# Kernel tuning notes

Hardware: AMD Instinct MI355X
Metric: run time of the kernel (lower is better)

The kernel has to match this reference:

```python
import jax, jax.numpy as jnp
import numpy as np

T, B = 8192, 4096
NEG_SLOPE = 0.01


def setup_inputs() -> dict:
    key = jax.random.key(0)
    k1, k2 = jax.random.split(key)
    input_seq = jax.random.randint(k1, (T, B), 0, 2, dtype=jnp.int32)
    delta = jax.random.normal(k2, (2,), dtype=jnp.float32)
    return {"input_seq": input_seq, "delta": delta}


def reference(input_seq, delta):
    # Per-step: counter += delta[inp]; output = leaky_relu(counter).
    # counter itself is never clamped, so this is exactly
    # leaky_relu(cumsum(delta[input_seq], axis=time)).
    steps = delta[input_seq]                 # [T, B] gather from 2-entry table
    counter = jnp.cumsum(steps, axis=0)      # [T, B] prefix sum over time
    return jnp.where(counter >= 0, counter, NEG_SLOPE * counter)
```

## Files before the change

### kernel.cpp

```cpp
#include <hip/hip_runtime.h>
#include <stdint.h>

#define T_DIM 8192
#define B_DIM 4096
#define WORDS (T_DIM / 32)
#define NSEG 16
#define CTILE 256
#define NEG_SLOPE 0.01f

__global__ __launch_bounds__(1024) void ka_pack(const int* __restrict__ in,
                                                uint32_t* __restrict__ bits,
                                                int* __restrict__ segTotal) {
    const int c4  = threadIdx.x & 63;
    const int rc  = threadIdx.x >> 6;
    const int col0 = blockIdx.x * CTILE + c4 * 4;
    const int wordrow = blockIdx.y * 16 + rc;
    const int row0 = wordrow * 32;

    const int4* __restrict__ inv = (const int4*)in;
    uint32_t b0 = 0, b1 = 0, b2 = 0, b3 = 0;
#pragma unroll
    for (int r = 0; r < 32; ++r) {
        int4 v = inv[((size_t)(row0 + r) * B_DIM + col0) >> 2];
        b0 |= ((uint32_t)v.x & 1u) << r;
        b1 |= ((uint32_t)v.y & 1u) << r;
        b2 |= ((uint32_t)v.z & 1u) << r;
        b3 |= ((uint32_t)v.w & 1u) << r;
    }

    ((uint4*)bits)[((size_t)wordrow * B_DIM + col0) >> 2] = make_uint4(b0, b1, b2, b3);

    __shared__ int4 lds[16 * 64];
    lds[rc * 64 + c4] = make_int4(__popc(b0), __popc(b1), __popc(b2), __popc(b3));
    __syncthreads();

    if (rc == 0) {
        int4 s = make_int4(0, 0, 0, 0);
#pragma unroll
        for (int i = 0; i < 16; ++i) {
            int4 v = lds[i * 64 + c4];
            s.x += v.x; s.y += v.y; s.z += v.z; s.w += v.w;
        }
        ((int4*)segTotal)[((size_t)blockIdx.y * B_DIM + col0) >> 2] = s;
    }
}

__global__ __launch_bounds__(1024) void kb_emit(const uint32_t* __restrict__ bits,
                                                const int* __restrict__ segTotal,
                                                const float* __restrict__ delta,
                                                float* __restrict__ out) {
    const int c4  = threadIdx.x & 63;
    const int rc  = threadIdx.x >> 6;
    const int col0 = blockIdx.x * CTILE + c4 * 4;
    const int seg = blockIdx.y;
    const int wordrow = seg * 16 + rc;
    const int row0 = wordrow * 32;

    uint4 w = ((const uint4*)bits)[((size_t)wordrow * B_DIM + col0) >> 2];

    __shared__ int4 lds[16 * 64];
    lds[rc * 64 + c4] = make_int4(__popc(w.x), __popc(w.y), __popc(w.z), __popc(w.w));

    int c0 = 0, c1 = 0, c2 = 0, c3 = 0;
    for (int s = 0; s < seg; ++s) {
        int4 v = ((const int4*)segTotal)[((size_t)s * B_DIM + col0) >> 2];
        c0 += v.x; c1 += v.y; c2 += v.z; c3 += v.w;
    }
    __syncthreads();

    for (int i = 0; i < rc; ++i) {
        int4 v = lds[i * 64 + c4];
        c0 += v.x; c1 += v.y; c2 += v.z; c3 += v.w;
    }

    const float d0 = delta[0];
    const float dd = delta[1] - d0;

    float4* __restrict__ outv = (float4*)out;
#pragma unroll
    for (int r = 0; r < 32; ++r) {
        const int t = row0 + r;
        const float tp = (float)(t + 1) * d0;
        c0 += (int)((w.x >> r) & 1u);
        c1 += (int)((w.y >> r) & 1u);
        c2 += (int)((w.z >> r) & 1u);
        c3 += (int)((w.w >> r) & 1u);
        float4 o;
        o.x = fmaf((float)c0, dd, tp);
        o.y = fmaf((float)c1, dd, tp);
        o.z = fmaf((float)c2, dd, tp);
        o.w = fmaf((float)c3, dd, tp);
        o.x = (o.x >= 0.0f) ? o.x : NEG_SLOPE * o.x;
        o.y = (o.y >= 0.0f) ? o.y : NEG_SLOPE * o.y;
        o.z = (o.z >= 0.0f) ? o.z : NEG_SLOPE * o.z;
        o.w = (o.w >= 0.0f) ? o.w : NEG_SLOPE * o.w;
        outv[((size_t)t * B_DIM + col0) >> 2] = o;
    }
}

extern "C" void kernel_launch(void* const* d_in, const int* in_sizes, int n_in,
                              void* d_out, int out_size, void* d_ws, size_t ws_size,
                              hipStream_t stream) {
    const int*   in    = (const int*)d_in[0];
    const float* delta = (const float*)d_in[1];
    float*       out   = (float*)d_out;

    uint32_t* bits     = (uint32_t*)d_ws;
    int*      segTotal = (int*)((char*)d_ws + (size_t)WORDS * B_DIM * 4);

    dim3 grid(B_DIM / CTILE, NSEG);
    dim3 block(1024);

    hipLaunchKernelGGL(ka_pack, grid, block, 0, stream, in, bits, segTotal);
    hipLaunchKernelGGL(kb_emit, grid, block, 0, stream, bits, segTotal, delta, out);
}
```

Measured before the change: 242.0 us.

## Fuse pack and emit kernels into one cooperative kernel with grid sync

```diff
diff --git a/kernel.cpp b/kernel.cpp
--- a/kernel.cpp
+++ b/kernel.cpp
@@ -1,20 +1,25 @@
 #include <hip/hip_runtime.h>
+#include <hip/hip_cooperative_groups.h>
 #include <stdint.h>
+
+namespace cg = cooperative_groups;
 
 #define T_DIM 8192
 #define B_DIM 4096
-#define WORDS (T_DIM / 32)
 #define NSEG 16
 #define CTILE 256
 #define NEG_SLOPE 0.01f
 
-__global__ __launch_bounds__(1024) void ka_pack(const int* __restrict__ in,
-                                                uint32_t* __restrict__ bits,
-                                                int* __restrict__ segTotal) {
+__global__ __launch_bounds__(1024, 1) void fused_counter(
+        const int* __restrict__ in,
+        const float* __restrict__ delta,
+        float* __restrict__ out,
+        int* __restrict__ segTotal) {
     const int c4  = threadIdx.x & 63;
     const int rc  = threadIdx.x >> 6;
     const int col0 = blockIdx.x * CTILE + c4 * 4;
-    const int wordrow = blockIdx.y * 16 + rc;
+    const int seg = blockIdx.y;
+    const int wordrow = seg * 16 + rc;
     const int row0 = wordrow * 32;
 
     const int4* __restrict__ inv = (const int4*)in;
@@ -28,8 +33,6 @@
         b3 |= ((uint32_t)v.w & 1u) << r;
     }
 
-    ((uint4*)bits)[((size_t)wordrow * B_DIM + col0) >> 2] = make_uint4(b0, b1, b2, b3);
-
     __shared__ int4 lds[16 * 64];
     lds[rc * 64 + c4] = make_int4(__popc(b0), __popc(b1), __popc(b2), __popc(b3));
     __syncthreads();
@@ -41,33 +44,16 @@
             int4 v = lds[i * 64 + c4];
             s.x += v.x; s.y += v.y; s.z += v.z; s.w += v.w;
         }
-        ((int4*)segTotal)[((size_t)blockIdx.y * B_DIM + col0) >> 2] = s;
+        ((int4*)segTotal)[((size_t)seg * B_DIM + col0) >> 2] = s;
     }
-}
 
-__global__ __launch_bounds__(1024) void kb_emit(const uint32_t* __restrict__ bits,
-                                                const int* __restrict__ segTotal,
-                                                const float* __restrict__ delta,
-                                                float* __restrict__ out) {
-    const int c4  = threadIdx.x & 63;
-    const int rc  = threadIdx.x >> 6;
-    const int col0 = blockIdx.x * CTILE + c4 * 4;
-    const int seg = blockIdx.y;
-    const int wordrow = seg * 16 + rc;
-    const int row0 = wordrow * 32;
-
-    uint4 w = ((const uint4*)bits)[((size_t)wordrow * B_DIM + col0) >> 2];
-
-    __shared__ int4 lds[16 * 64];
-    lds[rc * 64 + c4] = make_int4(__popc(w.x), __popc(w.y), __popc(w.z), __popc(w.w));
+    cg::this_grid().sync();
 
     int c0 = 0, c1 = 0, c2 = 0, c3 = 0;
     for (int s = 0; s < seg; ++s) {
         int4 v = ((const int4*)segTotal)[((size_t)s * B_DIM + col0) >> 2];
         c0 += v.x; c1 += v.y; c2 += v.z; c3 += v.w;
     }
-    __syncthreads();
-
     for (int i = 0; i < rc; ++i) {
         int4 v = lds[i * 64 + c4];
         c0 += v.x; c1 += v.y; c2 += v.z; c3 += v.w;
@@ -81,10 +67,10 @@
     for (int r = 0; r < 32; ++r) {
         const int t = row0 + r;
         const float tp = (float)(t + 1) * d0;
-        c0 += (int)((w.x >> r) & 1u);
-        c1 += (int)((w.y >> r) & 1u);
-        c2 += (int)((w.z >> r) & 1u);
-        c3 += (int)((w.w >> r) & 1u);
+        c0 += (int)((b0 >> r) & 1u);
+        c1 += (int)((b1 >> r) & 1u);
+        c2 += (int)((b2 >> r) & 1u);
+        c3 += (int)((b3 >> r) & 1u);
         float4 o;
         o.x = fmaf((float)c0, dd, tp);
         o.y = fmaf((float)c1, dd, tp);
@@ -104,13 +90,11 @@
     const int*   in    = (const int*)d_in[0];
     const float* delta = (const float*)d_in[1];
     float*       out   = (float*)d_out;
-
-    uint32_t* bits     = (uint32_t*)d_ws;
-    int*      segTotal = (int*)((char*)d_ws + (size_t)WORDS * B_DIM * 4);
+    int*         segTotal = (int*)d_ws;
 
     dim3 grid(B_DIM / CTILE, NSEG);
     dim3 block(1024);
 
-    hipLaunchKernelGGL(ka_pack, grid, block, 0, stream, in, bits, segTotal);
-    hipLaunchKernelGGL(kb_emit, grid, block, 0, stream, bits, segTotal, delta, out);
+    void* args[] = { (void*)&in, (void*)&delta, (void*)&out, (void*)&segTotal };
+    hipLaunchCooperativeKernel((void*)fused_counter, grid, block, args, 0, stream);
 }
```

Measured after the change: 363.7 us. +50.3%, slower.

## Split each bit-word across two threads, double segments, use nontemporal loads/stores

Applied to the files above, without the earlier changes.

```diff
diff --git a/kernel.cpp b/kernel.cpp
--- a/kernel.cpp
+++ b/kernel.cpp
@@ -3,63 +3,80 @@
 
 #define T_DIM 8192
 #define B_DIM 4096
-#define WORDS (T_DIM / 32)
-#define NSEG 16
+#define NSEG 32
 #define CTILE 256
 #define NEG_SLOPE 0.01f
 
-__global__ __launch_bounds__(1024) void ka_pack(const int* __restrict__ in,
-                                                uint32_t* __restrict__ bits,
-                                                int* __restrict__ segTotal) {
-    const int c4  = threadIdx.x & 63;
-    const int rc  = threadIdx.x >> 6;
+typedef int   ivec4 __attribute__((ext_vector_type(4)));
+typedef float fvec4 __attribute__((ext_vector_type(4)));
+
+
+__global__ __launch_bounds__(1024, 8) void ka_pack(const int* __restrict__ in,
+                                                   uint32_t* __restrict__ bits,
+                                                   int* __restrict__ segTotal) {
+    const int c4   = threadIdx.x & 63;
+    const int rr   = threadIdx.x >> 6;
+    const int wl   = rr >> 1;
+    const int half = rr & 1;
     const int col0 = blockIdx.x * CTILE + c4 * 4;
-    const int wordrow = blockIdx.y * 16 + rc;
-    const int row0 = wordrow * 32;
+    const int wordrow = blockIdx.y * 8 + wl;
+    const int row0 = wordrow * 32 + half * 16;
 
-    const int4* __restrict__ inv = (const int4*)in;
+    const ivec4* __restrict__ inv = (const ivec4*)in;
     uint32_t b0 = 0, b1 = 0, b2 = 0, b3 = 0;
 #pragma unroll
-    for (int r = 0; r < 32; ++r) {
-        int4 v = inv[((size_t)(row0 + r) * B_DIM + col0) >> 2];
+    for (int r = 0; r < 16; ++r) {
+        ivec4 v = __builtin_nontemporal_load(&inv[((size_t)(row0 + r) * B_DIM + col0) >> 2]);
         b0 |= ((uint32_t)v.x & 1u) << r;
         b1 |= ((uint32_t)v.y & 1u) << r;
         b2 |= ((uint32_t)v.z & 1u) << r;
         b3 |= ((uint32_t)v.w & 1u) << r;
     }
 
-    ((uint4*)bits)[((size_t)wordrow * B_DIM + col0) >> 2] = make_uint4(b0, b1, b2, b3);
-
-    __shared__ int4 lds[16 * 64];
-    lds[rc * 64 + c4] = make_int4(__popc(b0), __popc(b1), __popc(b2), __popc(b3));
+    __shared__ uint4 halves[16][64];
+    __shared__ int4  cnts[8][64];
+    halves[rr][c4] = make_uint4(b0, b1, b2, b3);
     __syncthreads();
 
-    if (rc == 0) {
+    if (half == 0) {
+        uint4 lo = halves[rr][c4];
+        uint4 hi = halves[rr + 1][c4];
+        uint4 w = make_uint4(lo.x | (hi.x << 16), lo.y | (hi.y << 16),
+                             lo.z | (hi.z << 16), lo.w | (hi.w << 16));
+        ((uint4*)bits)[((size_t)wordrow * B_DIM + col0) >> 2] = w;
+        cnts[wl][c4] = make_int4(__popc(w.x), __popc(w.y), __popc(w.z), __popc(w.w));
+    }
+    __syncthreads();
+
+    if (rr == 0) {
         int4 s = make_int4(0, 0, 0, 0);
 #pragma unroll
-        for (int i = 0; i < 16; ++i) {
-            int4 v = lds[i * 64 + c4];
+        for (int i = 0; i < 8; ++i) {
+            int4 v = cnts[i][c4];
             s.x += v.x; s.y += v.y; s.z += v.z; s.w += v.w;
         }
         ((int4*)segTotal)[((size_t)blockIdx.y * B_DIM + col0) >> 2] = s;
     }
 }
 
-__global__ __launch_bounds__(1024) void kb_emit(const uint32_t* __restrict__ bits,
-                                                const int* __restrict__ segTotal,
-                                                const float* __restrict__ delta,
-                                                float* __restrict__ out) {
-    const int c4  = threadIdx.x & 63;
-    const int rc  = threadIdx.x >> 6;
+__global__ __launch_bounds__(1024, 8) void kb_emit(const uint32_t* __restrict__ bits,
+                                                   const int* __restrict__ segTotal,
+                                                   const float* __restrict__ delta,
+                                                   float* __restrict__ out) {
+    const int c4   = threadIdx.x & 63;
+    const int rr   = threadIdx.x >> 6;
+    const int wl   = rr >> 1;
+    const int half = rr & 1;
     const int col0 = blockIdx.x * CTILE + c4 * 4;
-    const int seg = blockIdx.y;
-    const int wordrow = seg * 16 + rc;
-    const int row0 = wordrow * 32;
+    const int seg  = blockIdx.y;
+    const int wordrow = seg * 8 + wl;
+    const int row0 = wordrow * 32 + half * 16;
 
     uint4 w = ((const uint4*)bits)[((size_t)wordrow * B_DIM + col0) >> 2];
 
-    __shared__ int4 lds[16 * 64];
-    lds[rc * 64 + c4] = make_int4(__popc(w.x), __popc(w.y), __popc(w.z), __popc(w.w));
+    __shared__ int4 cnts[8][64];
+    if (half == 0)
+        cnts[wl][c4] = make_int4(__popc(w.x), __popc(w.y), __popc(w.z), __popc(w.w));
 
     int c0 = 0, c1 = 0, c2 = 0, c3 = 0;
     for (int s = 0; s < seg; ++s) {
@@ -68,33 +85,40 @@
     }
     __syncthreads();
 
-    for (int i = 0; i < rc; ++i) {
-        int4 v = lds[i * 64 + c4];
+    for (int i = 0; i < wl; ++i) {
+        int4 v = cnts[i][c4];
         c0 += v.x; c1 += v.y; c2 += v.z; c3 += v.w;
+    }
+    if (half) {
+        c0 += __popc(w.x & 0xFFFFu);
+        c1 += __popc(w.y & 0xFFFFu);
+        c2 += __popc(w.z & 0xFFFFu);
+        c3 += __popc(w.w & 0xFFFFu);
     }
 
     const float d0 = delta[0];
     const float dd = delta[1] - d0;
+    const int sh = half * 16;
 
-    float4* __restrict__ outv = (float4*)out;
+    fvec4* __restrict__ outv = (fvec4*)out;
 #pragma unroll
-    for (int r = 0; r < 32; ++r) {
+    for (int r = 0; r < 16; ++r) {
         const int t = row0 + r;
         const float tp = (float)(t + 1) * d0;
-        c0 += (int)((w.x >> r) & 1u);
-        c1 += (int)((w.y >> r) & 1u);
-        c2 += (int)((w.z >> r) & 1u);
-        c3 += (int)((w.w >> r) & 1u);
-        float4 o;
-        o.x = fmaf((float)c0, dd, tp);
-        o.y = fmaf((float)c1, dd, tp);
-        o.z = fmaf((float)c2, dd, tp);
-        o.w = fmaf((float)c3, dd, tp);
-        o.x = (o.x >= 0.0f) ? o.x : NEG_SLOPE * o.x;
-        o.y = (o.y >= 0.0f) ? o.y : NEG_SLOPE * o.y;
-        o.z = (o.z >= 0.0f) ? o.z : NEG_SLOPE * o.z;
-        o.w = (o.w >= 0.0f) ? o.w : NEG_SLOPE * o.w;
-        outv[((size_t)t * B_DIM + col0) >> 2] = o;
+        c0 += (int)((w.x >> (sh + r)) & 1u);
+        c1 += (int)((w.y >> (sh + r)) & 1u);
+        c2 += (int)((w.z >> (sh + r)) & 1u);
+        c3 += (int)((w.w >> (sh + r)) & 1u);
+        fvec4 o;
+        float ox = fmaf((float)c0, dd, tp);
+        float oy = fmaf((float)c1, dd, tp);
+        float oz = fmaf((float)c2, dd, tp);
+        float ow = fmaf((float)c3, dd, tp);
+        o.x = (ox >= 0.0f) ? ox : NEG_SLOPE * ox;
+        o.y = (oy >= 0.0f) ? oy : NEG_SLOPE * oy;
+        o.z = (oz >= 0.0f) ? oz : NEG_SLOPE * oz;
+        o.w = (ow >= 0.0f) ? ow : NEG_SLOPE * ow;
+        __builtin_nontemporal_store(o, &outv[((size_t)t * B_DIM + col0) >> 2]);
     }
 }
 
@@ -106,7 +130,7 @@
     float*       out   = (float*)d_out;
 
     uint32_t* bits     = (uint32_t*)d_ws;
-    int*      segTotal = (int*)((char*)d_ws + (size_t)WORDS * B_DIM * 4);
+    int*      segTotal = (int*)((char*)d_ws + (size_t)(T_DIM / 32) * B_DIM * 4);
 
     dim3 grid(B_DIM / CTILE, NSEG);
     dim3 block(1024);
```

After: 226.0 us. -6.6%, faster.
